# Optimization experiments

Measured on AMD Instinct MI355X. Metric: run time of the kernel, lower is better.

Reference implementation:

```python
import jax, jax.numpy as jnp
import numpy as np

PATCH_SIZES = (16, 32, 48, 64)
RES_IDX = (0, 1, 2, 3)  # min(int(s*4/3), 3) for s in 0..3
QUANT_RESI = 0.5
BETA = 0.25
D = 32      # embedding_dim == input channels
V = 2048    # vocab_size
G = 8       # GroupNorm groups
EPS = 1e-5


def conv3(x, w, b):
    y = jax.lax.conv_general_dilated(x, w, (1, 1), 'SAME', dimension_numbers=('NCHW', 'OIHW', 'NCHW'))
    return y + b[None, :, None, None]


def group_norm(x, gamma, beta):
    n, c, h, w = x.shape
    xr = x.reshape(n, G, c // G, h, w)
    mu = xr.mean(axis=(2, 3, 4), keepdims=True)
    var = xr.var(axis=(2, 3, 4), keepdims=True)
    xn = ((xr - mu) * jax.lax.rsqrt(var + EPS)).reshape(n, c, h, w)
    return xn * gamma[None, :, None, None] + beta[None, :, None, None]


def conv_block(x, w1, b1, gamma, beta, w2, b2):
    h = conv3(x, w1, b1)
    h = jax.nn.gelu(group_norm(h, gamma, beta), approximate=False)
    return conv3(h, w2, b2)


def _forward(x, emb, pw1, pb1, pg, pbt, pw2, pb2, rw1, rb1, rg, rbt, rw2, rb2):
    B, C, H, W = x.shape
    acc = jnp.zeros_like(x)
    total_loss = jnp.zeros((), x.dtype)
    idx_list = []
    for s, p in enumerate(PATCH_SIZES):
        nh, nw = H // p, W // p
        # unfold: non-overlapping patches -> (B*N, C, p, p), N row-major over (nh, nw)
        patches = (x - acc).reshape(B, C, nh, p, nw, p).transpose(0, 2, 4, 1, 3, 5).reshape(B * nh * nw, C, p, p)
        z = conv_block(patches, pw1[s], pb1[s], pg[s], pbt[s], pw2[s], pb2[s])
        zf = z.reshape(-1, D)  # raw row-major reshape, exactly as the torch code does
        d = (zf * zf).sum(1, keepdims=True) + (emb * emb).sum(1) - 2.0 * (zf @ emb.T)
        idx = jnp.argmin(d, axis=1)
        zq = emb[idx].reshape(z.shape)
        loss = jnp.mean((jax.lax.stop_gradient(zq) - z) ** 2) + BETA * jnp.mean((zq - jax.lax.stop_gradient(z)) ** 2)
        total_loss = total_loss + loss
        zq = z + jax.lax.stop_gradient(zq - z)  # straight-through estimator
        r = RES_IDX[s]
        zq = zq * (1.0 - QUANT_RESI) + conv_block(zq, rw1[r], rb1[r], rg[r], rbt[r], rw2[r], rb2[r]) * QUANT_RESI
        # fold: exact inverse of unfold (patch sizes divide H, W)
        decoded = zq.reshape(B, nh, nw, C, p, p).transpose(0, 3, 1, 4, 2, 5).reshape(B, C, H, W)
        acc = acc + decoded
        idx_list.append(idx.reshape(B, -1))
    return (jax.nn.sigmoid(acc), *idx_list, total_loss)


def setup_inputs() -> dict:
    key = jax.random.key(0)
    ks = jax.random.split(key, 4)
    S = len(PATCH_SIZES)
    x = jax.random.normal(ks[0], (1, D, 384, 384), dtype=jnp.float32)
    emb = jax.random.uniform(ks[1], (V, D), jnp.float32, -1.0 / V, 1.0 / V)

    def wset(k):
        k1, k2, k3, k4 = jax.random.split(k, 4)
        return (jax.random.normal(k1, (S, D, D, 3, 3), jnp.float32) * 0.05,
                jax.random.normal(k2, (S, D), jnp.float32) * 0.02,
                jnp.ones((S, D), jnp.float32),
                jnp.zeros((S, D), jnp.float32),
                jax.random.normal(k3, (S, D, D, 3, 3), jnp.float32) * 0.05,
                jax.random.normal(k4, (S, D), jnp.float32) * 0.02)

    pw1, pb1, pg, pbt, pw2, pb2 = wset(ks[2])
    rw1, rb1, rg, rbt, rw2, rb2 = wset(ks[3])
    return {"x": x, "emb": emb,
            "pw1": pw1, "pb1": pb1, "pg": pg, "pbt": pbt, "pw2": pw2, "pb2": pb2,
            "rw1": rw1, "rb1": rb1, "rg": rg, "rbt": rbt, "rw2": rw2, "rb2": rb2}


def reference(x, emb, pw1, pb1, pg, pbt, pw2, pb2, rw1, rb1, rg, rbt, rw2, rb2):
    return _forward(x, emb, pw1, pb1, pg, pbt, pw2, pb2, rw1, rb1, rg, rbt, rw2, rb2)
```

## Files before the change

kernel.cpp:

```cpp
#include <hip/hip_runtime.h>
#include <cmath>

#define WIDTH 384
#define HW 147456
#define CHW 4718592
#define NCH 32
#define NV 2048
#define NROWS 147456

typedef short vshort8 __attribute__((ext_vector_type(8)));
typedef float vfloat4 __attribute__((ext_vector_type(4)));

__device__ inline unsigned short bf_split(float x, float& back) {
  unsigned int b; __builtin_memcpy(&b, &x, 4);
  unsigned int r = (b + 0x7FFFu + ((b >> 16) & 1u)) >> 16;
  unsigned int bb = r << 16; float f; __builtin_memcpy(&f, &bb, 4);
  back = f; return (unsigned short)r;
}

template <int SQ>
__device__ float np_pw(const float* a, int n, float mu) {
  if (n < 8) {
    float res = 0.0f;
    for (int i = 0; i < n; i++) {
      float v = a[i];
      if (SQ) { float d = __fsub_rn(v, mu); v = __fmul_rn(d, d); }
      res = __fadd_rn(res, v);
    }
    return res;
  }
  if (n <= 128) {
    float r[8];
#pragma unroll
    for (int j = 0; j < 8; j++) {
      float v = a[j];
      if (SQ) { float d = __fsub_rn(v, mu); v = __fmul_rn(d, d); }
      r[j] = v;
    }
    int i;
    for (i = 8; i + 8 <= n; i += 8) {
#pragma unroll
      for (int j = 0; j < 8; j++) {
        float v = a[i + j];
        if (SQ) { float d = __fsub_rn(v, mu); v = __fmul_rn(d, d); }
        r[j] = __fadd_rn(r[j], v);
      }
    }
    float res = __fadd_rn(__fadd_rn(__fadd_rn(r[0], r[1]), __fadd_rn(r[2], r[3])),
                          __fadd_rn(__fadd_rn(r[4], r[5]), __fadd_rn(r[6], r[7])));
    for (; i < n; i++) {
      float v = a[i];
      if (SQ) { float d = __fsub_rn(v, mu); v = __fmul_rn(d, d); }
      res = __fadd_rn(res, v);
    }
    return res;
  }
  int n2 = n / 2; n2 -= n2 % 8;
  return __fadd_rn(np_pw<SQ>(a, n2, mu), np_pw<SQ>(a + n2, n - n2, mu));
}

__global__ __launch_bounds__(256) void prep_kernel(
    const float* __restrict__ pw1, const float* __restrict__ pw2,
    const float* __restrict__ rw1, const float* __restrict__ rw2,
    const float* __restrict__ emb, float* __restrict__ wt, float* __restrict__ ee,
    unsigned short* __restrict__ eh, unsigned short* __restrict__ el) {
  int t = blockIdx.x * 256 + threadIdx.x;
  if (t < 147456) {
    int layer = t / 9216, r = t % 9216;
    int k = r / 32, co = r % 32;
    int set = layer >> 2, s = layer & 3;
    const float* src = set == 0 ? pw1 : set == 1 ? pw2 : set == 2 ? rw1 : rw2;
    wt[t] = src[s * 9216 + co * 288 + k];
  } else if (t < 147456 + NV) {
    int v = t - 147456;
    const float* e = emb + v * 32;
    float r[8];
#pragma unroll
    for (int j = 0; j < 8; j++) r[j] = __fmul_rn(e[j], e[j]);
#pragma unroll
    for (int i = 8; i < 32; i += 8)
#pragma unroll
      for (int j = 0; j < 8; j++) r[j] = __fadd_rn(r[j], __fmul_rn(e[i + j], e[i + j]));
    ee[v] = __fadd_rn(__fadd_rn(__fadd_rn(r[0], r[1]), __fadd_rn(r[2], r[3])),
                      __fadd_rn(__fadd_rn(r[4], r[5]), __fadd_rn(r[6], r[7])));
  } else if (t < 147456 + NV + 65536) {
    int idx = t - 147456 - NV;
    float x = emb[idx], hb;
    eh[idx] = bf_split(x, hb);
    float lb;
    el[idx] = bf_split(__fsub_rn(x, hb), lb);
  }
}

template <int MODE>
__global__ __launch_bounds__(192, 3) void conv32_kernel(
    const float* __restrict__ in, const float* __restrict__ x,
    const float* __restrict__ accin, float* __restrict__ outb,
    const float* __restrict__ zqb, float* __restrict__ acc,
    const float* __restrict__ wt, const float* __restrict__ bias, int p, int nw) {
  int t = blockIdx.x * 192 + threadIdx.x;
  int pp = p * p;
  int px = t % p; int t1 = t / p;
  int py = t1 % p;
  int n  = t1 / p;
  int i = n / nw, j = n % nw;

  int off[9]; bool msk[9];
#pragma unroll
  for (int dy = 0; dy < 3; dy++) {
    int ly = py + dy - 1;
    bool vy = (unsigned)ly < (unsigned)p;
    int cy = vy ? ly : 0;
#pragma unroll
    for (int dx = 0; dx < 3; dx++) {
      int lx = px + dx - 1;
      bool vx = (unsigned)lx < (unsigned)p;
      int cx = vx ? lx : 0;
      msk[dy * 3 + dx] = vy && vx;
      if (MODE == 1) off[dy * 3 + dx] = (i * p + cy) * WIDTH + (j * p + cx);
      else           off[dy * 3 + dx] = cy * p + cx;
    }
  }

  const float* pin = (MODE == 1) ? nullptr : in + (size_t)n * NCH * pp;

  float a[NCH];
#pragma unroll
  for (int co = 0; co < NCH; co++) a[co] = 0.0f;

  float tv[9], tn[9];
#pragma unroll
  for (int k = 0; k < 9; k++) {
    float v;
    if (MODE == 1) {
      size_t ad = (size_t)off[k];
      v = __fsub_rn(x[ad], accin[ad]);
    } else {
      v = pin[off[k]];
    }
    tv[k] = msk[k] ? v : 0.0f;
  }

  for (int ci = 0; ci < NCH; ci++) {
    if (ci + 1 < NCH) {
#pragma unroll
      for (int k = 0; k < 9; k++) {
        float v;
        if (MODE == 1) {
          size_t ad = (size_t)(ci + 1) * HW + off[k];
          v = __fsub_rn(x[ad], accin[ad]);
        } else {
          v = pin[(size_t)(ci + 1) * pp + off[k]];
        }
        tn[k] = msk[k] ? v : 0.0f;
      }
    }
    const float* wp = wt + ci * 288;
#pragma unroll
    for (int k = 0; k < 9; k++) {
#pragma unroll
      for (int co = 0; co < NCH; co++)
        a[co] = fmaf(tv[k], wp[k * 32 + co], a[co]);
    }
#pragma unroll
    for (int k = 0; k < 9; k++) tv[k] = tn[k];
  }

#pragma unroll
  for (int co = 0; co < NCH; co++) {
    float r = __fadd_rn(a[co], bias[co]);
    if (MODE == 2) {
      size_t img = (size_t)co * HW + (size_t)(i * p + py) * WIDTH + (j * p + px);
      size_t pt  = (size_t)n * NCH * pp + (size_t)co * pp + (size_t)py * p + px;
      float dec = __fadd_rn(__fmul_rn(zqb[pt], 0.5f), __fmul_rn(r, 0.5f));
      acc[img] = __fadd_rn(acc[img], dec);
    } else {
      outb[(size_t)n * NCH * pp + (size_t)co * pp + (size_t)py * p + px] = r;
    }
  }
}

__global__ __launch_bounds__(64) void gn_stats_kernel(
    const float* __restrict__ buf, float2* __restrict__ stats,
    int p, int C, int chunk) {
  int tid = threadIdx.x;
  int gpw = 64 / C;
  int gi = tid / C, cl = tid % C;
  int grp = blockIdx.x * gpw + gi;
  int pp = p * p, ne = 4 * pp;
  const float* base = buf + ((size_t)(grp >> 3) * NCH + (size_t)(grp & 7) * 4) * pp
                      + (size_t)cl * chunk;

  float s = np_pw<0>(base, chunk, 0.0f);
  for (int m = 1; m < C; m <<= 1) s = __fadd_rn(s, __shfl_xor(s, m, 64));
  float mu = __fdiv_rn(s, (float)ne);

  float s2 = np_pw<1>(base, chunk, mu);
  for (int m = 1; m < C; m <<= 1) s2 = __fadd_rn(s2, __shfl_xor(s2, m, 64));

  if (cl == 0) {
    float var = __fdiv_rn(s2, (float)ne);
    float rs = __fdiv_rn(1.0f, __fsqrt_rn(__fadd_rn(var, 1e-5f)));
    stats[grp] = make_float2(mu, rs);
  }
}

__global__ __launch_bounds__(256) void gn_gelu_kernel(
    float* __restrict__ buf, const float2* __restrict__ stats,
    const float* __restrict__ gamma, const float* __restrict__ beta, int p) {
  int t = blockIdx.x * 256 + threadIdx.x;
  int pp = p * p;
  int t2 = t / pp;
  int c = t2 % NCH;
  int n = t2 / NCH;
  float2 st = stats[n * 8 + (c >> 2)];
  float v = __fadd_rn(__fmul_rn(__fmul_rn(__fsub_rn(buf[t], st.x), st.y), gamma[c]), beta[c]);
  float tt = __fdiv_rn(v, 1.41421356237309504880f);
  float e = (float)erf((double)tt);
  buf[t] = __fmul_rn(__fmul_rn(0.5f, v), __fadd_rn(1.0f, e));
}

__global__ __launch_bounds__(192) void zsplit_kernel(
    const float* __restrict__ z, unsigned short* __restrict__ zh,
    unsigned short* __restrict__ zl, float* __restrict__ zz) {
  int r = blockIdx.x * 192 + threadIdx.x;
  const float* zr = z + (size_t)r * 32;
  float zv[32];
#pragma unroll
  for (int q = 0; q < 32; q++) zv[q] = zr[q];

  float rr[8];
#pragma unroll
  for (int j = 0; j < 8; j++) rr[j] = __fmul_rn(zv[j], zv[j]);
#pragma unroll
  for (int i = 8; i < 32; i += 8)
#pragma unroll
    for (int j = 0; j < 8; j++) rr[j] = __fadd_rn(rr[j], __fmul_rn(zv[i + j], zv[i + j]));
  zz[r] = __fadd_rn(__fadd_rn(__fadd_rn(rr[0], rr[1]), __fadd_rn(rr[2], rr[3])),
                    __fadd_rn(__fadd_rn(rr[4], rr[5]), __fadd_rn(rr[6], rr[7])));

  unsigned short hbits[32], lbits[32];
#pragma unroll
  for (int q = 0; q < 32; q++) {
    float hb;
    hbits[q] = bf_split(zv[q], hb);
    float lb;
    lbits[q] = bf_split(__fsub_rn(zv[q], hb), lb);
  }
#pragma unroll
  for (int c = 0; c < 4; c++) {
    vshort8 hv, lv;
#pragma unroll
    for (int j = 0; j < 8; j++) { hv[j] = (short)hbits[c * 8 + j]; lv[j] = (short)lbits[c * 8 + j]; }
    *(vshort8*)(zh + (size_t)r * 32 + c * 8) = hv;
    *(vshort8*)(zl + (size_t)r * 32 + c * 8) = lv;
  }
}

__global__ __launch_bounds__(576, 5) void gemm_min_kernel(
    const unsigned short* __restrict__ ZH, const unsigned short* __restrict__ ZL,
    const float* __restrict__ ZZ,
    const unsigned short* __restrict__ EH, const unsigned short* __restrict__ EL,
    const float* __restrict__ EE,
    float* __restrict__ BD, float* __restrict__ B2, int* __restrict__ I1) {
  __shared__ float ee_l[2048];
  int tid = threadIdx.x;
  for (int i = tid; i < 2048; i += 576) ee_l[i] = EE[i];
  __syncthreads();

  int wid = tid / 64, lane = tid & 63;
  int t0 = blockIdx.x * 18 + wid * 2;
  int lr = lane & 15, lg = lane >> 4;

  vshort8 azh0 = *(const vshort8*)(ZH + (size_t)(t0 * 16 + lr) * 32 + 8 * lg);
  vshort8 azl0 = *(const vshort8*)(ZL + (size_t)(t0 * 16 + lr) * 32 + 8 * lg);
  vshort8 azh1 = *(const vshort8*)(ZH + (size_t)((t0 + 1) * 16 + lr) * 32 + 8 * lg);
  vshort8 azl1 = *(const vshort8*)(ZL + (size_t)((t0 + 1) * 16 + lr) * 32 + 8 * lg);
  float zzv[8];
#pragma unroll
  for (int r = 0; r < 4; r++) {
    zzv[r]     = ZZ[t0 * 16 + 4 * lg + r];
    zzv[4 + r] = ZZ[(t0 + 1) * 16 + 4 * lg + r];
  }

  float b1[8], b2[8]; int i1[8];
#pragma unroll
  for (int r = 0; r < 8; r++) { b1[r] = 3.402823466e+38f; b2[r] = 3.402823466e+38f; i1[r] = 0; }

  vshort8 nbeh = *(const vshort8*)(EH + (size_t)lr * 32 + 8 * lg);
  vshort8 nbel = *(const vshort8*)(EL + (size_t)lr * 32 + 8 * lg);

  for (int ct = 0; ct < 128; ct++) {
    vshort8 beh = nbeh, bel = nbel;
    if (ct + 1 < 128) {
      nbeh = *(const vshort8*)(EH + (size_t)((ct + 1) * 16 + lr) * 32 + 8 * lg);
      nbel = *(const vshort8*)(EL + (size_t)((ct + 1) * 16 + lr) * 32 + 8 * lg);
    }
    vfloat4 acc0 = {0.0f, 0.0f, 0.0f, 0.0f};
    acc0 = __builtin_amdgcn_mfma_f32_16x16x32_bf16(azh0, beh, acc0, 0, 0, 0);
    acc0 = __builtin_amdgcn_mfma_f32_16x16x32_bf16(azh0, bel, acc0, 0, 0, 0);
    acc0 = __builtin_amdgcn_mfma_f32_16x16x32_bf16(azl0, beh, acc0, 0, 0, 0);
    vfloat4 acc1 = {0.0f, 0.0f, 0.0f, 0.0f};
    acc1 = __builtin_amdgcn_mfma_f32_16x16x32_bf16(azh1, beh, acc1, 0, 0, 0);
    acc1 = __builtin_amdgcn_mfma_f32_16x16x32_bf16(azh1, bel, acc1, 0, 0, 0);
    acc1 = __builtin_amdgcn_mfma_f32_16x16x32_bf16(azl1, beh, acc1, 0, 0, 0);
    int col = ct * 16 + lr;
    float eev = ee_l[col];
#pragma unroll
    for (int r = 0; r < 4; r++) {
      float d = (zzv[r] + eev) - 2.0f * acc0[r];
      if (d < b1[r]) { b2[r] = b1[r]; b1[r] = d; i1[r] = col; }
      else b2[r] = fminf(b2[r], d);
      float d1 = (zzv[4 + r] + eev) - 2.0f * acc1[r];
      if (d1 < b1[4 + r]) { b2[4 + r] = b1[4 + r]; b1[4 + r] = d1; i1[4 + r] = col; }
      else b2[4 + r] = fminf(b2[4 + r], d1);
    }
  }

  for (int m = 1; m < 16; m <<= 1) {
#pragma unroll
    for (int r = 0; r < 8; r++) {
      float ob1 = __shfl_xor(b1[r], m, 64);
      int   oi1 = __shfl_xor(i1[r], m, 64);
      float ob2 = __shfl_xor(b2[r], m, 64);
      bool aw = (b1[r] < ob1) || (b1[r] == ob1 && i1[r] < oi1);
      float lo = aw ? ob1 : b1[r];
      b1[r] = aw ? b1[r] : ob1;
      i1[r] = aw ? i1[r] : oi1;
      b2[r] = fminf(fminf(b2[r], ob2), lo);
    }
  }

  if (lr == 0) {
#pragma unroll
    for (int r = 0; r < 4; r++) {
      int row0 = t0 * 16 + 4 * lg + r;
      BD[row0] = b1[r]; B2[row0] = b2[r]; I1[row0] = i1[r];
      int row1 = (t0 + 1) * 16 + 4 * lg + r;
      BD[row1] = b1[4 + r]; B2[row1] = b2[4 + r]; I1[row1] = i1[4 + r];
    }
  }
}

__global__ __launch_bounds__(256) void epilogue_kernel(
    const float* __restrict__ z, const float* __restrict__ emb,
    const float* __restrict__ BD, const float* __restrict__ B2,
    const int* __restrict__ I1, float* __restrict__ zq,
    float* __restrict__ idxout, double* __restrict__ ssep,
    int* __restrict__ list, int* __restrict__ cnt) {
  int t = blockIdx.x * 256 + threadIdx.x;
  int row = t >> 2, part = t & 3;
  float bd = BD[row];
  int bi = I1[row];
  float margin = __fadd_rn(1.0e-6f, __fmul_rn(5.0e-7f, fabsf(bd)));
  bool flagged = (B2[row] - bd) <= margin;
  if (flagged && part == 0) {
    int i = atomicAdd(cnt, 1);
    list[i] = row;
  }
  const float4* ep = (const float4*)(emb + (size_t)bi * 32 + part * 8);
  const float4* zp = (const float4*)(z + (size_t)row * 32 + part * 8);
  float4* qp = (float4*)(zq + (size_t)row * 32 + part * 8);
  float4 e0 = ep[0], e1 = ep[1];
  float4 z0 = zp[0], z1 = zp[1];
  qp[0] = e0; qp[1] = e1;
  double sse = 0.0, d;
  d = (double)e0.x - (double)z0.x; sse += d * d;
  d = (double)e0.y - (double)z0.y; sse += d * d;
  d = (double)e0.z - (double)z0.z; sse += d * d;
  d = (double)e0.w - (double)z0.w; sse += d * d;
  d = (double)e1.x - (double)z1.x; sse += d * d;
  d = (double)e1.y - (double)z1.y; sse += d * d;
  d = (double)e1.z - (double)z1.z; sse += d * d;
  d = (double)e1.w - (double)z1.w; sse += d * d;
  ssep[t] = sse;
  if (part == 0) idxout[row] = (float)bi;
}

__global__ __launch_bounds__(64) void rescore_kernel(
    const float* __restrict__ z, const float* __restrict__ emb,
    const float* __restrict__ EE, const float* __restrict__ ZZ,
    float* __restrict__ zq, float* __restrict__ idxout,
    double* __restrict__ ssep, const int* __restrict__ list,
    const int* __restrict__ cnt) {
  int lane = threadIdx.x;
  int n = *cnt;
  for (int i = blockIdx.x; i < n; i += gridDim.x) {
    int row = list[i];
    const float* zp = z + (size_t)row * 32;
    float zb[32];
#pragma unroll
    for (int q = 0; q < 32; q++) zb[q] = zp[q];
    float zzb = ZZ[row];
    float bestd = 3.402823466e+38f;
    int bestv = NV;
    for (int k = 0; k < 32; k++) {
      int v = lane + 64 * k;
      const float* e0 = emb + (size_t)v * 32;
      float m = 0.0f;
#pragma unroll
      for (int q = 0; q < 32; q++) m = fmaf(zb[q], e0[q], m);
      float d = __fsub_rn(__fadd_rn(zzb, EE[v]), __fmul_rn(2.0f, m));
      if (d < bestd) { bestd = d; bestv = v; }
    }
    for (int mm = 1; mm < 64; mm <<= 1) {
      float od = __shfl_xor(bestd, mm, 64);
      int ov = __shfl_xor(bestv, mm, 64);
      if (od < bestd || (od == bestd && ov < bestv)) { bestd = od; bestv = ov; }
    }
    if (lane < 32) zq[(size_t)row * 32 + lane] = emb[bestv * 32 + lane];
    if (lane < 4) {
      const float* ep = emb + bestv * 32 + lane * 8;
      const float* zr = z + (size_t)row * 32 + lane * 8;
      double sse = 0.0;
#pragma unroll
      for (int q = 0; q < 8; q++) {
        double dd = (double)ep[q] - (double)zr[q];
        sse += dd * dd;
      }
      ssep[row * 4 + lane] = sse;
    }
    if (lane == 0) idxout[row] = (float)bestv;
  }
}

__global__ __launch_bounds__(256) void ssered_kernel(
    const double* __restrict__ ssep, double* __restrict__ part) {
  __shared__ double red[256];
  int t = blockIdx.x * 256 + threadIdx.x;
  const double* b = ssep + (size_t)t * 4;
  red[threadIdx.x] = ((b[0] + b[1]) + (b[2] + b[3]));
  __syncthreads();
  for (int st = 128; st > 0; st >>= 1) {
    if (threadIdx.x < st) red[threadIdx.x] += red[threadIdx.x + st];
    __syncthreads();
  }
  if (threadIdx.x == 0) part[blockIdx.x] = red[0];
}

__global__ __launch_bounds__(256) void sigmoid_kernel(
    const float* __restrict__ acc, float* __restrict__ out) {
  int t = blockIdx.x * 256 + threadIdx.x;
  out[t] = (float)(1.0 / (1.0 + exp(-(double)acc[t])));
}

__global__ void loss_kernel(const double* __restrict__ part, float* __restrict__ out) {
  double tot = 0.0;
  for (int s = 0; s < 4; s++) {
    double sse = 0.0;
    for (int b = 0; b < 576; b++) sse += part[s * 1024 + b];
    tot += 1.25 * sse / 4718592.0;
  }
  out[0] = (float)tot;
}

extern "C" void kernel_launch(void* const* d_in, const int* in_sizes, int n_in,
                              void* d_out, int out_size, void* d_ws, size_t ws_size,
                              hipStream_t stream) {
  const float* X   = (const float*)d_in[0];
  const float* EMB = (const float*)d_in[1];
  const float* PW1 = (const float*)d_in[2];
  const float* PB1 = (const float*)d_in[3];
  const float* PG  = (const float*)d_in[4];
  const float* PBT = (const float*)d_in[5];
  const float* PW2 = (const float*)d_in[6];
  const float* PB2 = (const float*)d_in[7];
  const float* RW1 = (const float*)d_in[8];
  const float* RB1 = (const float*)d_in[9];
  const float* RG  = (const float*)d_in[10];
  const float* RBT = (const float*)d_in[11];
  const float* RW2 = (const float*)d_in[12];
  const float* RB2 = (const float*)d_in[13];
  float* out = (float*)d_out;

  char* w = (char*)d_ws;
  float*          EE    = (float*)(w);
  float*          WT    = (float*)(w + 8192UL);
  unsigned short* EH    = (unsigned short*)(w + 598016UL);
  unsigned short* EL    = (unsigned short*)(w + 729088UL);
  float2*         STATS = (float2*)(w + 860160UL);
  double*         PART  = (double*)(w + 897024UL);
  float*          ZZ    = (float*)(w + 929792UL);
  float*          BD    = (float*)(w + 1519616UL);
  float*          B2    = (float*)(w + 2109440UL);
  int*            I1    = (int*)(w + 2699264UL);
  unsigned short* ZH    = (unsigned short*)(w + 3289088UL);
  unsigned short* ZL    = (unsigned short*)(w + 12726272UL);
  float*          P     = (float*)(w + 22163456UL);
  float*          H     = (float*)(w + 41037824UL);
  float*          ACC   = (float*)(w + 59912192UL);
  int*            CNT   = (int*)(w + 78786560UL);
  int*            LIST  = (int*)(w + 78786624UL);
  double*         SSEP  = (double*)(w + 79376448UL);

  hipMemsetAsync(ACC, 0, 18874368UL, stream);
  hipMemsetAsync(CNT, 0, 64UL, stream);
  prep_kernel<<<840, 256, 0, stream>>>(PW1, PW2, RW1, RW2, EMB, WT, EE, EH, EL);

  const int PS[4] = {16, 32, 48, 64};
  for (int s = 0; s < 4; s++) {
    int p = PS[s], nw = 384 / p, N = nw * nw;
    int C = (p == 16) ? 8 : (p == 32) ? 32 : 64;
    int chunk = (4 * p * p) / C;
    int gblocks = (N * 8 * C) / 64;
    const float* wt_p1 = WT + (0 * 4 + s) * 9216;
    const float* wt_p2 = WT + (1 * 4 + s) * 9216;
    const float* wt_r1 = WT + (2 * 4 + s) * 9216;
    const float* wt_r2 = WT + (3 * 4 + s) * 9216;

    conv32_kernel<1><<<768, 192, 0, stream>>>(nullptr, X, ACC, H, nullptr, nullptr,
                                              wt_p1, PB1 + s * 32, p, nw);
    gn_stats_kernel<<<gblocks, 64, 0, stream>>>(H, STATS, p, C, chunk);
    gn_gelu_kernel<<<18432, 256, 0, stream>>>(H, STATS, PG + s * 32, PBT + s * 32, p);
    conv32_kernel<0><<<768, 192, 0, stream>>>(H, nullptr, nullptr, P, nullptr, nullptr,
                                              wt_p2, PB2 + s * 32, p, nw);
    zsplit_kernel<<<768, 192, 0, stream>>>(P, ZH, ZL, ZZ);
    gemm_min_kernel<<<512, 576, 0, stream>>>(ZH, ZL, ZZ, EH, EL, EE, BD, B2, I1);
    epilogue_kernel<<<2304, 256, 0, stream>>>(P, EMB, BD, B2, I1, H,
                                              out + 4718592 + s * 147456, SSEP,
                                              LIST, CNT + s);
    rescore_kernel<<<1024, 64, 0, stream>>>(P, EMB, EE, ZZ, H,
                                            out + 4718592 + s * 147456, SSEP,
                                            LIST, CNT + s);
    ssered_kernel<<<576, 256, 0, stream>>>(SSEP, PART + s * 1024);
    conv32_kernel<0><<<768, 192, 0, stream>>>(H, nullptr, nullptr, P, nullptr, nullptr,
                                              wt_r1, RB1 + s * 32, p, nw);
    gn_stats_kernel<<<gblocks, 64, 0, stream>>>(P, STATS, p, C, chunk);
    gn_gelu_kernel<<<18432, 256, 0, stream>>>(P, STATS, RG + s * 32, RBT + s * 32, p);
    conv32_kernel<2><<<768, 192, 0, stream>>>(P, nullptr, nullptr, nullptr, H, ACC,
                                              wt_r2, RB2 + s * 32, p, nw);
  }

  sigmoid_kernel<<<18432, 256, 0, stream>>>(ACC, out);
  loss_kernel<<<1, 1, 0, stream>>>(PART, out + 5308416);
}
```

Baseline: 2.071 ms.

## Fuse z bf16 split into GEMM-argmin and stage conv weights in LDS

Removes the separate zsplit kernel: the gemm_min kernel now loads fp32 z directly, computes the row squared norms via cross-lane shuffles, and performs the bf16 hi/lo split in registers. The rescore kernel recomputes the row norm instead of reading a stored ZZ buffer, and the workspace layout shrinks accordingly. Separately, the conv kernel copies its 9216-float weight slice into 36 KB of shared memory per block before the channel loop, replacing global/scalar weight reads with LDS reads. The LDS staging adds a sync and may reduce occupancy under the 192x3 launch bounds. The shuffle-based norm keeps the same summation order as the old kernel.

```diff
diff --git a/kernel.cpp b/kernel.cpp
--- a/kernel.cpp
+++ b/kernel.cpp
@@ -98,6 +98,10 @@
     const float* __restrict__ accin, float* __restrict__ outb,
     const float* __restrict__ zqb, float* __restrict__ acc,
     const float* __restrict__ wt, const float* __restrict__ bias, int p, int nw) {
+  __shared__ float wl[9216];
+  for (int i = threadIdx.x; i < 9216; i += 192) wl[i] = wt[i];
+  __syncthreads();
+
   int t = blockIdx.x * 192 + threadIdx.x;
   int pp = p * p;
   int px = t % p; int t1 = t / p;
@@ -155,7 +159,7 @@
         tn[k] = msk[k] ? v : 0.0f;
       }
     }
-    const float* wp = wt + ci * 288;
+    const float* wp = wl + ci * 288;
 #pragma unroll
     for (int k = 0; k < 9; k++) {
 #pragma unroll
@@ -220,46 +224,8 @@
   buf[t] = __fmul_rn(__fmul_rn(0.5f, v), __fadd_rn(1.0f, e));
 }
 
-__global__ __launch_bounds__(192) void zsplit_kernel(
-    const float* __restrict__ z, unsigned short* __restrict__ zh,
-    unsigned short* __restrict__ zl, float* __restrict__ zz) {
-  int r = blockIdx.x * 192 + threadIdx.x;
-  const float* zr = z + (size_t)r * 32;
-  float zv[32];
-#pragma unroll
-  for (int q = 0; q < 32; q++) zv[q] = zr[q];
-
-  float rr[8];
-#pragma unroll
-  for (int j = 0; j < 8; j++) rr[j] = __fmul_rn(zv[j], zv[j]);
-#pragma unroll
-  for (int i = 8; i < 32; i += 8)
-#pragma unroll
-    for (int j = 0; j < 8; j++) rr[j] = __fadd_rn(rr[j], __fmul_rn(zv[i + j], zv[i + j]));
-  zz[r] = __fadd_rn(__fadd_rn(__fadd_rn(rr[0], rr[1]), __fadd_rn(rr[2], rr[3])),
-                    __fadd_rn(__fadd_rn(rr[4], rr[5]), __fadd_rn(rr[6], rr[7])));
-
-  unsigned short hbits[32], lbits[32];
-#pragma unroll
-  for (int q = 0; q < 32; q++) {
-    float hb;
-    hbits[q] = bf_split(zv[q], hb);
-    float lb;
-    lbits[q] = bf_split(__fsub_rn(zv[q], hb), lb);
-  }
-#pragma unroll
-  for (int c = 0; c < 4; c++) {
-    vshort8 hv, lv;
-#pragma unroll
-    for (int j = 0; j < 8; j++) { hv[j] = (short)hbits[c * 8 + j]; lv[j] = (short)lbits[c * 8 + j]; }
-    *(vshort8*)(zh + (size_t)r * 32 + c * 8) = hv;
-    *(vshort8*)(zl + (size_t)r * 32 + c * 8) = lv;
-  }
-}
-
 __global__ __launch_bounds__(576, 5) void gemm_min_kernel(
-    const unsigned short* __restrict__ ZH, const unsigned short* __restrict__ ZL,
-    const float* __restrict__ ZZ,
+    const float* __restrict__ z,
     const unsigned short* __restrict__ EH, const unsigned short* __restrict__ EL,
     const float* __restrict__ EE,
     float* __restrict__ BD, float* __restrict__ B2, int* __restrict__ I1) {
@@ -272,15 +238,52 @@
   int t0 = blockIdx.x * 18 + wid * 2;
   int lr = lane & 15, lg = lane >> 4;
 
-  vshort8 azh0 = *(const vshort8*)(ZH + (size_t)(t0 * 16 + lr) * 32 + 8 * lg);
-  vshort8 azl0 = *(const vshort8*)(ZL + (size_t)(t0 * 16 + lr) * 32 + 8 * lg);
-  vshort8 azh1 = *(const vshort8*)(ZH + (size_t)((t0 + 1) * 16 + lr) * 32 + 8 * lg);
-  vshort8 azl1 = *(const vshort8*)(ZL + (size_t)((t0 + 1) * 16 + lr) * 32 + 8 * lg);
+  float za0[8], za1[8];
+  {
+    const float4* zp0 = (const float4*)(z + (size_t)(t0 * 16 + lr) * 32 + 8 * lg);
+    const float4* zp1 = (const float4*)(z + (size_t)((t0 + 1) * 16 + lr) * 32 + 8 * lg);
+    float4 c0 = zp0[0], c1 = zp0[1], d0 = zp1[0], d1 = zp1[1];
+    za0[0]=c0.x; za0[1]=c0.y; za0[2]=c0.z; za0[3]=c0.w;
+    za0[4]=c1.x; za0[5]=c1.y; za0[6]=c1.z; za0[7]=c1.w;
+    za1[0]=d0.x; za1[1]=d0.y; za1[2]=d0.z; za1[3]=d0.w;
+    za1[4]=d1.x; za1[5]=d1.y; za1[6]=d1.z; za1[7]=d1.w;
+  }
+
+  float zz0, zz1;
+  {
+    float r0[8], r1[8];
+#pragma unroll
+    for (int j = 0; j < 8; j++) {
+      float p0 = __fmul_rn(za0[j], za0[j]);
+      float p1 = __fmul_rn(za1[j], za1[j]);
+      float a0 = __shfl(p0, lr, 64),      a1 = __shfl(p0, 16 + lr, 64);
+      float a2 = __shfl(p0, 32 + lr, 64), a3 = __shfl(p0, 48 + lr, 64);
+      r0[j] = __fadd_rn(__fadd_rn(__fadd_rn(a0, a1), a2), a3);
+      float b0 = __shfl(p1, lr, 64),      b1 = __shfl(p1, 16 + lr, 64);
+      float b2_ = __shfl(p1, 32 + lr, 64), b3 = __shfl(p1, 48 + lr, 64);
+      r1[j] = __fadd_rn(__fadd_rn(__fadd_rn(b0, b1), b2_), b3);
+    }
+    zz0 = __fadd_rn(__fadd_rn(__fadd_rn(r0[0], r0[1]), __fadd_rn(r0[2], r0[3])),
+                    __fadd_rn(__fadd_rn(r0[4], r0[5]), __fadd_rn(r0[6], r0[7])));
+    zz1 = __fadd_rn(__fadd_rn(__fadd_rn(r1[0], r1[1]), __fadd_rn(r1[2], r1[3])),
+                    __fadd_rn(__fadd_rn(r1[4], r1[5]), __fadd_rn(r1[6], r1[7])));
+  }
   float zzv[8];
 #pragma unroll
   for (int r = 0; r < 4; r++) {
-    zzv[r]     = ZZ[t0 * 16 + 4 * lg + r];
-    zzv[4 + r] = ZZ[(t0 + 1) * 16 + 4 * lg + r];
+    zzv[r]     = __shfl(zz0, 4 * lg + r, 64);
+    zzv[4 + r] = __shfl(zz1, 4 * lg + r, 64);
+  }
+
+  vshort8 azh0, azl0, azh1, azl1;
+#pragma unroll
+  for (int j = 0; j < 8; j++) {
+    float hb;
+    azh0[j] = (short)bf_split(za0[j], hb);
+    float lb;
+    azl0[j] = (short)bf_split(__fsub_rn(za0[j], hb), lb);
+    azh1[j] = (short)bf_split(za1[j], hb);
+    azl1[j] = (short)bf_split(__fsub_rn(za1[j], hb), lb);
   }
 
   float b1[8], b2[8]; int i1[8];
@@ -379,7 +382,7 @@
 
 __global__ __launch_bounds__(64) void rescore_kernel(
     const float* __restrict__ z, const float* __restrict__ emb,
-    const float* __restrict__ EE, const float* __restrict__ ZZ,
+    const float* __restrict__ EE,
     float* __restrict__ zq, float* __restrict__ idxout,
     double* __restrict__ ssep, const int* __restrict__ list,
     const int* __restrict__ cnt) {
@@ -391,7 +394,15 @@
     float zb[32];
 #pragma unroll
     for (int q = 0; q < 32; q++) zb[q] = zp[q];
-    float zzb = ZZ[row];
+    float rr[8];
+#pragma unroll
+    for (int j = 0; j < 8; j++) rr[j] = __fmul_rn(zb[j], zb[j]);
+#pragma unroll
+    for (int ii = 8; ii < 32; ii += 8)
+#pragma unroll
+      for (int j = 0; j < 8; j++) rr[j] = __fadd_rn(rr[j], __fmul_rn(zb[ii + j], zb[ii + j]));
+    float zzb = __fadd_rn(__fadd_rn(__fadd_rn(rr[0], rr[1]), __fadd_rn(rr[2], rr[3])),
+                          __fadd_rn(__fadd_rn(rr[4], rr[5]), __fadd_rn(rr[6], rr[7])));
     float bestd = 3.402823466e+38f;
     int bestv = NV;
     for (int k = 0; k < 32; k++) {
@@ -480,18 +491,15 @@
   unsigned short* EL    = (unsigned short*)(w + 729088UL);
   float2*         STATS = (float2*)(w + 860160UL);
   double*         PART  = (double*)(w + 897024UL);
-  float*          ZZ    = (float*)(w + 929792UL);
-  float*          BD    = (float*)(w + 1519616UL);
-  float*          B2    = (float*)(w + 2109440UL);
-  int*            I1    = (int*)(w + 2699264UL);
-  unsigned short* ZH    = (unsigned short*)(w + 3289088UL);
-  unsigned short* ZL    = (unsigned short*)(w + 12726272UL);
-  float*          P     = (float*)(w + 22163456UL);
-  float*          H     = (float*)(w + 41037824UL);
-  float*          ACC   = (float*)(w + 59912192UL);
-  int*            CNT   = (int*)(w + 78786560UL);
-  int*            LIST  = (int*)(w + 78786624UL);
-  double*         SSEP  = (double*)(w + 79376448UL);
+  float*          BD    = (float*)(w + 929792UL);
+  float*          B2    = (float*)(w + 1519616UL);
+  int*            I1    = (int*)(w + 2109440UL);
+  float*          P     = (float*)(w + 2699264UL);
+  float*          H     = (float*)(w + 21573632UL);
+  float*          ACC   = (float*)(w + 40448000UL);
+  int*            CNT   = (int*)(w + 59322368UL);
+  int*            LIST  = (int*)(w + 59322432UL);
+  double*         SSEP  = (double*)(w + 59912256UL);
 
   hipMemsetAsync(ACC, 0, 18874368UL, stream);
   hipMemsetAsync(CNT, 0, 64UL, stream);
@@ -514,12 +522,11 @@
     gn_gelu_kernel<<<18432, 256, 0, stream>>>(H, STATS, PG + s * 32, PBT + s * 32, p);
     conv32_kernel<0><<<768, 192, 0, stream>>>(H, nullptr, nullptr, P, nullptr, nullptr,
                                               wt_p2, PB2 + s * 32, p, nw);
-    zsplit_kernel<<<768, 192, 0, stream>>>(P, ZH, ZL, ZZ);
-    gemm_min_kernel<<<512, 576, 0, stream>>>(ZH, ZL, ZZ, EH, EL, EE, BD, B2, I1);
+    gemm_min_kernel<<<512, 576, 0, stream>>>(P, EH, EL, EE, BD, B2, I1);
     epilogue_kernel<<<2304, 256, 0, stream>>>(P, EMB, BD, B2, I1, H,
                                               out + 4718592 + s * 147456, SSEP,
                                               LIST, CNT + s);
-    rescore_kernel<<<1024, 64, 0, stream>>>(P, EMB, EE, ZZ, H,
+    rescore_kernel<<<1024, 64, 0, stream>>>(P, EMB, EE, H,
                                             out + 4718592 + s * 147456, SSEP,
                                             LIST, CNT + s);
     ssered_kernel<<<576, 256, 0, stream>>>(SSEP, PART + s * 1024);
```

Result: slower. 2.258 ms (+9.0%).
